# Kernel optimization log

Hardware: AMD Instinct MI355X
Metric: run time of the kernel (lower is better)

Reference implementation:

```python
import jax, jax.numpy as jnp
import numpy as np

INF = 100000000.0
TOPK = 27


def _box_iou(a, b):
    # a: [N,4] (x1,y1,x2,y2), b: [G,4] -> iou [N,G]
    area_a = (a[:, 2] - a[:, 0]) * (a[:, 3] - a[:, 1])
    area_b = (b[:, 2] - b[:, 0]) * (b[:, 3] - b[:, 1])
    lt = jnp.maximum(a[:, None, :2], b[None, :, :2])
    rb = jnp.minimum(a[:, None, 2:], b[None, :, 2:])
    wh = jnp.clip(rb - lt, 0.0)
    inter = wh[..., 0] * wh[..., 1]
    union = area_a[:, None] + area_b[None, :] - inter
    return inter / union, union


def _assign_one(anchors, gts, tokens):
    # anchors [N,4], gts [G,4], tokens [G,T]
    N = anchors.shape[0]
    G = gts.shape[0]
    ious, _ = _box_iou(anchors, gts)  # [N,G]

    a_cx = (anchors[:, 2] + anchors[:, 0]) * 0.5
    a_cy = (anchors[:, 3] + anchors[:, 1]) * 0.5
    g_cx = (gts[:, 2] + gts[:, 0]) * 0.5
    g_cy = (gts[:, 3] + gts[:, 1]) * 0.5

    # pairwise center distance [N,G]
    dist = jnp.sqrt((a_cx[:, None] - g_cx[None, :]) ** 2 +
                    (a_cy[:, None] - g_cy[None, :]) ** 2)

    # topk nearest anchors per gt (smallest distance) -> idxs [G,TOPK]
    _, topk_idxs = jax.lax.top_k(-dist.T, TOPK)

    # candidate ious [G,TOPK]
    cand = jnp.take_along_axis(ious.T, topk_idxs, axis=1)
    iou_mean = cand.mean(axis=1)
    iou_std = cand.std(axis=1, ddof=1)  # torch.std is unbiased
    is_pos = cand >= (iou_mean + iou_std)[:, None]

    # center-inside-gt check [G,TOPK]
    ax = a_cx[topk_idxs]
    ay = a_cy[topk_idxs]
    l = ax - gts[:, 0:1]
    t = ay - gts[:, 1:2]
    r = gts[:, 2:3] - ax
    b = gts[:, 3:4] - ay
    is_in_gts = jnp.minimum(jnp.minimum(l, t), jnp.minimum(r, b)) > 0.01
    is_pos = is_pos & is_in_gts

    # scatter candidate ious into flat [G*N] buffer of -INF (indices are unique)
    flat_idx = (jnp.arange(G)[:, None] * N + topk_idxs).reshape(-1)
    vals = ious.T.reshape(-1)[flat_idx]
    scat = jnp.where(is_pos.reshape(-1), vals, -INF)
    ious_inf = jnp.full((G * N,), -INF, dtype=ious.dtype).at[flat_idx].set(scat)
    ious_inf = ious_inf.reshape(G, N).T  # [N,G]

    anchors_to_gt_values = ious_inf.max(axis=1)          # [N]
    anchors_to_gt_indexs = ious_inf.argmax(axis=1)       # [N]

    matched_gts = gts[anchors_to_gt_indexs]              # [N,4]

    T = tokens.shape[1]
    unmatched = jnp.zeros((T,), tokens.dtype).at[-1].set(1.0)
    token_labels = jnp.where((anchors_to_gt_values == -INF)[:, None],
                             unmatched[None, :],
                             tokens[anchors_to_gt_indexs])  # [N,T]
    return anchors_to_gt_values, anchors_to_gt_indexs, matched_gts, token_labels


def setup_inputs() -> dict:
    key = jax.random.key(0)
    k1, k2, k3, k4, k5 = jax.random.split(key, 5)
    B, N, G, T = 8, 100000, 64, 256
    # anchors: valid x1<x2, y1<y2 boxes on a ~1024px canvas
    a_c = jax.random.uniform(k1, (B, N, 2), jnp.float32, 0.0, 1024.0)
    a_wh = jax.random.uniform(k2, (B, N, 2), jnp.float32, 8.0, 128.0)
    anchor_boxes = jnp.concatenate([a_c - a_wh / 2, a_c + a_wh / 2], axis=-1)
    g_c = jax.random.uniform(k3, (B, G, 2), jnp.float32, 0.0, 1024.0)
    g_wh = jax.random.uniform(k4, (B, G, 2), jnp.float32, 64.0, 512.0)
    gt_boxes = jnp.concatenate([g_c - g_wh / 2, g_c + g_wh / 2], axis=-1)
    token_map = jax.random.uniform(k5, (B, G, T), jnp.float32)
    return {"anchor_boxes": anchor_boxes, "gt_boxes": gt_boxes,
            "token_map": token_map}


def reference(anchor_boxes, gt_boxes, token_map):
    return jax.vmap(_assign_one)(anchor_boxes, gt_boxes, token_map)
```

## Files before the change

kernel.cpp:

```cpp
#include <hip/hip_runtime.h>
#include <cstdint>

constexpr int B = 8, N = 100000, G = 64, T = 256, TOPK = 27;
constexpr int BN = B * N;
constexpr int CAP = 2048;
constexpr int TOKEN_BLOCKS = 2048;
#define NEG_INF_VAL (-100000000.0f)

typedef float v4f __attribute__((ext_vector_type(4)));

__global__ __launch_bounds__(256) void atss_centers_kernel(
    const float* __restrict__ anchors, float2* __restrict__ ctr,
    unsigned long long* __restrict__ best)
{
#pragma clang fp contract(off)
  int i = blockIdx.x * 256 + threadIdx.x;
  if (i < BN) {
    float4 ab = ((const float4*)anchors)[i];
    ctr[i] = make_float2((ab.z + ab.x) * 0.5f, (ab.w + ab.y) * 0.5f);
    best[i] = 0ULL;
  }
}

__global__ __launch_bounds__(1024) void atss_assign_kernel(
    const float* __restrict__ anchors,
    const float2* __restrict__ ctr,
    const float* __restrict__ gts,
    unsigned long long* __restrict__ best)
{
#pragma clang fp contract(off)
  __shared__ float s_d[CAP];
  __shared__ int   s_i[CAP];
  __shared__ int   s_cnt;
  __shared__ int   s_sel[TOPK];
  __shared__ float s_iou[TOPK];
  __shared__ int   s_in[TOPK];
  __shared__ float s_thresh;

  const int bid = blockIdx.x;
  const int bg  = (bid & 7) * (B * G / 8) + (bid >> 3);
  const int b   = bg / G;
  const int g   = bg % G;
  const int tid = threadIdx.x;

  const float4 gbox = ((const float4*)gts)[bg];
  const float g_cx = (gbox.z + gbox.x) * 0.5f;
  const float g_cy = (gbox.w + gbox.y) * 0.5f;

  const float4*  abase = (const float4*)(anchors + (size_t)b * N * 4);
  const float2*  cbase = ctr + (size_t)b * N;
  const float4*  c4    = (const float4*)cbase;

  float thr2 = 24.0f * 24.0f;
  int M = 0;
  for (int attempt = 0; attempt < 8; ++attempt) {
    if (tid == 0) s_cnt = 0;
    __syncthreads();
    for (int m = tid; m < N / 4; m += 1024) {
      float4 ca = c4[2 * m];
      float4 cb = c4[2 * m + 1];
      float dx0 = ca.x - g_cx, dy0 = ca.y - g_cy;
      float d20 = __fmul_rn(dx0, dx0) + __fmul_rn(dy0, dy0);
      float dx1 = ca.z - g_cx, dy1 = ca.w - g_cy;
      float d21 = __fmul_rn(dx1, dx1) + __fmul_rn(dy1, dy1);
      float dx2 = cb.x - g_cx, dy2 = cb.y - g_cy;
      float d22 = __fmul_rn(dx2, dx2) + __fmul_rn(dy2, dy2);
      float dx3 = cb.z - g_cx, dy3 = cb.w - g_cy;
      float d23 = __fmul_rn(dx3, dx3) + __fmul_rn(dy3, dy3);
      if (d20 < thr2) {
        int p = atomicAdd(&s_cnt, 1);
        if (p < CAP) { s_d[p] = __fsqrt_rn(d20); s_i[p] = 4 * m; }
      }
      if (d21 < thr2) {
        int p = atomicAdd(&s_cnt, 1);
        if (p < CAP) { s_d[p] = __fsqrt_rn(d21); s_i[p] = 4 * m + 1; }
      }
      if (d22 < thr2) {
        int p = atomicAdd(&s_cnt, 1);
        if (p < CAP) { s_d[p] = __fsqrt_rn(d22); s_i[p] = 4 * m + 2; }
      }
      if (d23 < thr2) {
        int p = atomicAdd(&s_cnt, 1);
        if (p < CAP) { s_d[p] = __fsqrt_rn(d23); s_i[p] = 4 * m + 3; }
      }
    }
    __syncthreads();
    int cnt = s_cnt;
    __syncthreads();
    if (cnt >= TOPK && cnt <= CAP) { M = cnt; break; }
    thr2 = (cnt < TOPK) ? thr2 * 16.0f : thr2 * 0.25f;
  }

  for (int s = tid; s < M; s += 1024) {
    unsigned long long pk_s =
        ((unsigned long long)__float_as_uint(s_d[s]) << 20) |
        (unsigned long long)(unsigned)s_i[s];
    int rank = 0;
    for (int j = 0; j < M; ++j) {
      unsigned long long pk_j =
          ((unsigned long long)__float_as_uint(s_d[j]) << 20) |
          (unsigned long long)(unsigned)s_i[j];
      rank += (pk_j < pk_s) ? 1 : 0;
    }
    if (rank < TOPK) s_sel[rank] = s_i[s];
  }
  __syncthreads();

  if (tid < TOPK) {
    int a = s_sel[tid];
    float4 ab = abase[a];
    float area_a = __fmul_rn(ab.z - ab.x, ab.w - ab.y);
    float area_b = __fmul_rn(gbox.z - gbox.x, gbox.w - gbox.y);
    float ltx = fmaxf(ab.x, gbox.x), lty = fmaxf(ab.y, gbox.y);
    float rbx = fminf(ab.z, gbox.z), rby = fminf(ab.w, gbox.w);
    float w = fmaxf(rbx - ltx, 0.0f), h = fmaxf(rby - lty, 0.0f);
    float inter = __fmul_rn(w, h);
    float uni = (area_a + area_b) - inter;
    s_iou[tid] = inter / uni;
    float acx = (ab.z + ab.x) * 0.5f, acy = (ab.w + ab.y) * 0.5f;
    float l = acx - gbox.x, t = acy - gbox.y;
    float r = gbox.z - acx, bt = gbox.w - acy;
    float mn = fminf(fminf(l, t), fminf(r, bt));
    s_in[tid] = (mn > 0.01f) ? 1 : 0;
  }
  __syncthreads();

  if (tid == 0) {
    float sum = 0.0f;
    for (int k = 0; k < TOPK; ++k) sum += s_iou[k];
    float mean = sum / (float)TOPK;
    float vs = 0.0f;
    for (int k = 0; k < TOPK; ++k) {
      float d = s_iou[k] - mean;
      vs += __fmul_rn(d, d);
    }
    float sd = __fsqrt_rn(vs / (float)(TOPK - 1));
    s_thresh = mean + sd;
  }
  __syncthreads();

  if (tid < TOPK) {
    float iou = s_iou[tid];
    if (s_in[tid] && iou >= s_thresh) {
      unsigned long long pk =
          ((unsigned long long)__float_as_uint(iou) << 32) |
          (unsigned long long)(0xFFFFFFFFu - (unsigned)g);
      atomicMax(&best[(size_t)b * N + s_sel[tid]], pk);
    }
  }
}

__global__ __launch_bounds__(256) void atss_scalar_write_kernel(
    const unsigned long long* __restrict__ best,
    const float* __restrict__ gts,
    float* __restrict__ out)
{
  float* __restrict__ out_val = out;
  float* __restrict__ out_idx = out + (size_t)BN;
  float* __restrict__ out_mg  = out + (size_t)2 * BN;

  const int i = blockIdx.x * 256 + threadIdx.x;
  unsigned long long p = best[i];
  const int b_ = i / N;
  int g = 0;
  float val = NEG_INF_VAL;
  if (p != 0ULL) {
    g   = (int)(0xFFFFFFFFu - (unsigned)(p & 0xFFFFFFFFULL));
    val = __uint_as_float((unsigned)(p >> 32));
  }
  const int row = b_ * G + g;
  out_val[i] = val;
  out_idx[i] = (float)g;
  ((v4f*)out_mg)[i] = ((const v4f*)gts)[row];
}

__global__ __launch_bounds__(256) void atss_token_kernel(
    const unsigned long long* __restrict__ best,
    const float* __restrict__ tokens,
    float* __restrict__ out)
{
  float* __restrict__ out_tok = out + (size_t)6 * BN;
  const int lane = threadIdx.x & 63;
  const int NW   = TOKEN_BLOCKS * 4;
  int row = (blockIdx.x << 2) | (threadIdx.x >> 6);
  const v4f* tok4 = (const v4f*)tokens;

  unsigned long long p = best[row];
  while (true) {
    const int nrow = row + NW;
    unsigned long long pn = (nrow < BN) ? best[nrow] : 0ULL;
    v4f t;
    if (p != 0ULL) {
      const int b_ = row / N;
      const int g  = (int)(0xFFFFFFFFu - (unsigned)(p & 0xFFFFFFFFULL));
      t = tok4[(size_t)(b_ * G + g) * 64 + lane];
    } else {
      t = (v4f){0.0f, 0.0f, 0.0f, 0.0f};
      if (lane == 63) t.w = 1.0f;
    }
    ((v4f*)(out_tok + (size_t)row * T))[lane] = t;
    if (nrow >= BN) break;
    row = nrow;
    p = pn;
  }
}

extern "C" void kernel_launch(void* const* d_in, const int* in_sizes, int n_in,
                              void* d_out, int out_size, void* d_ws, size_t ws_size,
                              hipStream_t stream) {
  const float* anchors = (const float*)d_in[0];
  const float* gts     = (const float*)d_in[1];
  const float* tokens  = (const float*)d_in[2];
  float* out = (float*)d_out;

  unsigned long long* best = (unsigned long long*)d_ws;
  float2* ctr = (float2*)((char*)d_ws + sizeof(unsigned long long) * (size_t)BN);

  atss_centers_kernel<<<BN / 256, 256, 0, stream>>>(anchors, ctr, best);
  atss_assign_kernel<<<B * G, 1024, 0, stream>>>(anchors, ctr, gts, best);
  atss_scalar_write_kernel<<<BN / 256, 256, 0, stream>>>(best, gts, out);
  atss_token_kernel<<<TOKEN_BLOCKS, 256, 0, stream>>>(best, tokens, out);
}
```

Before: 846.5 us.

## Process two GT boxes per block to share anchor-center loads

Each assign block now handles two ground-truth boxes, scanning the anchor centers once and testing each center against both boxes, with separate candidate buffers and adaptive thresholds. This halves the number of center-array passes across the grid, cutting global memory traffic for the distance scan. In exchange the grid has only 256 blocks, fewer than the number of compute units, so parallelism drops. The per-box candidate capacity is reduced to fit two buffers in shared memory, which raises the chance of extra threshold retries.

```diff
diff --git a/kernel.cpp b/kernel.cpp
--- a/kernel.cpp
+++ b/kernel.cpp
@@ -3,7 +3,8 @@
 
 constexpr int B = 8, N = 100000, G = 64, T = 256, TOPK = 27;
 constexpr int BN = B * N;
-constexpr int CAP = 2048;
+constexpr int CAP = 1536;
+constexpr int GPB = 2;
 constexpr int TOKEN_BLOCKS = 2048;
 #define NEG_INF_VAL (-100000000.0f)
 
@@ -29,124 +30,142 @@
     unsigned long long* __restrict__ best)
 {
 #pragma clang fp contract(off)
-  __shared__ float s_d[CAP];
-  __shared__ int   s_i[CAP];
-  __shared__ int   s_cnt;
-  __shared__ int   s_sel[TOPK];
-  __shared__ float s_iou[TOPK];
-  __shared__ int   s_in[TOPK];
+  __shared__ float s_d[GPB][CAP];
+  __shared__ int   s_i[GPB][CAP];
+  __shared__ int   s_cnt[GPB];
+  __shared__ int   s_sel[GPB][TOPK];
+  __shared__ float s_iou[GPB][TOPK];
+  __shared__ int   s_in[GPB][TOPK];
   __shared__ float s_thresh;
 
   const int bid = blockIdx.x;
-  const int bg  = (bid & 7) * (B * G / 8) + (bid >> 3);
-  const int b   = bg / G;
-  const int g   = bg % G;
+  const int p   = (bid & 7) * 32 + (bid >> 3);
+  const int b   = p >> 5;
+  const int g0  = (p & 31) * 2;
+  const int bg0 = b * G + g0;
   const int tid = threadIdx.x;
 
-  const float4 gbox = ((const float4*)gts)[bg];
-  const float g_cx = (gbox.z + gbox.x) * 0.5f;
-  const float g_cy = (gbox.w + gbox.y) * 0.5f;
-
-  const float4*  abase = (const float4*)(anchors + (size_t)b * N * 4);
-  const float2*  cbase = ctr + (size_t)b * N;
-  const float4*  c4    = (const float4*)cbase;
-
-  float thr2 = 24.0f * 24.0f;
-  int M = 0;
-  for (int attempt = 0; attempt < 8; ++attempt) {
-    if (tid == 0) s_cnt = 0;
-    __syncthreads();
+  const float4 gb0 = ((const float4*)gts)[bg0];
+  const float4 gb1 = ((const float4*)gts)[bg0 + 1];
+  const float gcx0 = (gb0.z + gb0.x) * 0.5f, gcy0 = (gb0.w + gb0.y) * 0.5f;
+  const float gcx1 = (gb1.z + gb1.x) * 0.5f, gcy1 = (gb1.w + gb1.y) * 0.5f;
+
+  const float4* abase = (const float4*)(anchors + (size_t)b * N * 4);
+  const float4* c4    = (const float4*)(ctr + (size_t)b * N);
+
+  float thr2_0 = 576.0f, thr2_1 = 576.0f;
+  int M0 = -1, M1 = -1;
+  for (int attempt = 0; attempt < 8 && (M0 < 0 || M1 < 0); ++attempt) {
+    if (tid == 0 && M0 < 0) s_cnt[0] = 0;
+    if (tid == 1 && M1 < 0) s_cnt[1] = 0;
+    __syncthreads();
+    const bool a0 = (M0 < 0), a1 = (M1 < 0);
+
+#define ATSS_TEST(cx, cy, idx)                                                \
+  do {                                                                        \
+    if (a0) {                                                                 \
+      float dx = (cx) - gcx0, dy = (cy) - gcy0;                               \
+      float d2 = __fmul_rn(dx, dx) + __fmul_rn(dy, dy);                       \
+      if (d2 < thr2_0) {                                                      \
+        int q_ = atomicAdd(&s_cnt[0], 1);                                     \
+        if (q_ < CAP) { s_d[0][q_] = __fsqrt_rn(d2); s_i[0][q_] = (idx); }    \
+      }                                                                       \
+    }                                                                         \
+    if (a1) {                                                                 \
+      float dx = (cx) - gcx1, dy = (cy) - gcy1;                               \
+      float d2 = __fmul_rn(dx, dx) + __fmul_rn(dy, dy);                       \
+      if (d2 < thr2_1) {                                                      \
+        int q_ = atomicAdd(&s_cnt[1], 1);                                     \
+        if (q_ < CAP) { s_d[1][q_] = __fsqrt_rn(d2); s_i[1][q_] = (idx); }    \
+      }                                                                       \
+    }                                                                         \
+  } while (0)
+
     for (int m = tid; m < N / 4; m += 1024) {
       float4 ca = c4[2 * m];
       float4 cb = c4[2 * m + 1];
-      float dx0 = ca.x - g_cx, dy0 = ca.y - g_cy;
-      float d20 = __fmul_rn(dx0, dx0) + __fmul_rn(dy0, dy0);
-      float dx1 = ca.z - g_cx, dy1 = ca.w - g_cy;
-      float d21 = __fmul_rn(dx1, dx1) + __fmul_rn(dy1, dy1);
-      float dx2 = cb.x - g_cx, dy2 = cb.y - g_cy;
-      float d22 = __fmul_rn(dx2, dx2) + __fmul_rn(dy2, dy2);
-      float dx3 = cb.z - g_cx, dy3 = cb.w - g_cy;
-      float d23 = __fmul_rn(dx3, dx3) + __fmul_rn(dy3, dy3);
-      if (d20 < thr2) {
-        int p = atomicAdd(&s_cnt, 1);
-        if (p < CAP) { s_d[p] = __fsqrt_rn(d20); s_i[p] = 4 * m; }
+      ATSS_TEST(ca.x, ca.y, 4 * m);
+      ATSS_TEST(ca.z, ca.w, 4 * m + 1);
+      ATSS_TEST(cb.x, cb.y, 4 * m + 2);
+      ATSS_TEST(cb.z, cb.w, 4 * m + 3);
+    }
+#undef ATSS_TEST
+    __syncthreads();
+    const int c0 = s_cnt[0], c1 = s_cnt[1];
+    __syncthreads();
+    if (M0 < 0) {
+      if (c0 >= TOPK && c0 <= CAP) M0 = c0;
+      else thr2_0 *= (c0 < TOPK) ? 16.0f : 0.25f;
+    }
+    if (M1 < 0) {
+      if (c1 >= TOPK && c1 <= CAP) M1 = c1;
+      else thr2_1 *= (c1 < TOPK) ? 16.0f : 0.25f;
+    }
+  }
+
+  for (int q = 0; q < GPB; ++q) {
+    const int M = (q == 0) ? M0 : M1;
+    const float4 gbox = (q == 0) ? gb0 : gb1;
+    const int g = g0 + q;
+
+    for (int s = tid; s < M; s += 1024) {
+      unsigned long long pk_s =
+          ((unsigned long long)__float_as_uint(s_d[q][s]) << 20) |
+          (unsigned long long)(unsigned)s_i[q][s];
+      int rank = 0;
+      for (int j = 0; j < M; ++j) {
+        unsigned long long pk_j =
+            ((unsigned long long)__float_as_uint(s_d[q][j]) << 20) |
+            (unsigned long long)(unsigned)s_i[q][j];
+        rank += (pk_j < pk_s) ? 1 : 0;
       }
-      if (d21 < thr2) {
-        int p = atomicAdd(&s_cnt, 1);
-        if (p < CAP) { s_d[p] = __fsqrt_rn(d21); s_i[p] = 4 * m + 1; }
+      if (rank < TOPK) s_sel[q][rank] = s_i[q][s];
+    }
+    __syncthreads();
+
+    if (tid < TOPK) {
+      int a = s_sel[q][tid];
+      float4 ab = abase[a];
+      float area_a = __fmul_rn(ab.z - ab.x, ab.w - ab.y);
+      float area_b = __fmul_rn(gbox.z - gbox.x, gbox.w - gbox.y);
+      float ltx = fmaxf(ab.x, gbox.x), lty = fmaxf(ab.y, gbox.y);
+      float rbx = fminf(ab.z, gbox.z), rby = fminf(ab.w, gbox.w);
+      float w = fmaxf(rbx - ltx, 0.0f), h = fmaxf(rby - lty, 0.0f);
+      float inter = __fmul_rn(w, h);
+      float uni = (area_a + area_b) - inter;
+      s_iou[q][tid] = inter / uni;
+      float acx = (ab.z + ab.x) * 0.5f, acy = (ab.w + ab.y) * 0.5f;
+      float l = acx - gbox.x, t = acy - gbox.y;
+      float r = gbox.z - acx, bt = gbox.w - acy;
+      float mn = fminf(fminf(l, t), fminf(r, bt));
+      s_in[q][tid] = (mn > 0.01f) ? 1 : 0;
+    }
+    __syncthreads();
+
+    if (tid == 0) {
+      float sum = 0.0f;
+      for (int k = 0; k < TOPK; ++k) sum += s_iou[q][k];
+      float mean = sum / (float)TOPK;
+      float vs = 0.0f;
+      for (int k = 0; k < TOPK; ++k) {
+        float d = s_iou[q][k] - mean;
+        vs += __fmul_rn(d, d);
       }
-      if (d22 < thr2) {
-        int p = atomicAdd(&s_cnt, 1);
-        if (p < CAP) { s_d[p] = __fsqrt_rn(d22); s_i[p] = 4 * m + 2; }
+      float sd = __fsqrt_rn(vs / (float)(TOPK - 1));
+      s_thresh = mean + sd;
+    }
+    __syncthreads();
+
+    if (tid < TOPK) {
+      float iou = s_iou[q][tid];
+      if (s_in[q][tid] && iou >= s_thresh) {
+        unsigned long long pk =
+            ((unsigned long long)__float_as_uint(iou) << 32) |
+            (unsigned long long)(0xFFFFFFFFu - (unsigned)g);
+        atomicMax(&best[(size_t)b * N + s_sel[q][tid]], pk);
       }
-      if (d23 < thr2) {
-        int p = atomicAdd(&s_cnt, 1);
-        if (p < CAP) { s_d[p] = __fsqrt_rn(d23); s_i[p] = 4 * m + 3; }
-      }
-    }
-    __syncthreads();
-    int cnt = s_cnt;
-    __syncthreads();
-    if (cnt >= TOPK && cnt <= CAP) { M = cnt; break; }
-    thr2 = (cnt < TOPK) ? thr2 * 16.0f : thr2 * 0.25f;
-  }
-
-  for (int s = tid; s < M; s += 1024) {
-    unsigned long long pk_s =
-        ((unsigned long long)__float_as_uint(s_d[s]) << 20) |
-        (unsigned long long)(unsigned)s_i[s];
-    int rank = 0;
-    for (int j = 0; j < M; ++j) {
-      unsigned long long pk_j =
-          ((unsigned long long)__float_as_uint(s_d[j]) << 20) |
-          (unsigned long long)(unsigned)s_i[j];
-      rank += (pk_j < pk_s) ? 1 : 0;
-    }
-    if (rank < TOPK) s_sel[rank] = s_i[s];
-  }
-  __syncthreads();
-
-  if (tid < TOPK) {
-    int a = s_sel[tid];
-    float4 ab = abase[a];
-    float area_a = __fmul_rn(ab.z - ab.x, ab.w - ab.y);
-    float area_b = __fmul_rn(gbox.z - gbox.x, gbox.w - gbox.y);
-    float ltx = fmaxf(ab.x, gbox.x), lty = fmaxf(ab.y, gbox.y);
-    float rbx = fminf(ab.z, gbox.z), rby = fminf(ab.w, gbox.w);
-    float w = fmaxf(rbx - ltx, 0.0f), h = fmaxf(rby - lty, 0.0f);
-    float inter = __fmul_rn(w, h);
-    float uni = (area_a + area_b) - inter;
-    s_iou[tid] = inter / uni;
-    float acx = (ab.z + ab.x) * 0.5f, acy = (ab.w + ab.y) * 0.5f;
-    float l = acx - gbox.x, t = acy - gbox.y;
-    float r = gbox.z - acx, bt = gbox.w - acy;
-    float mn = fminf(fminf(l, t), fminf(r, bt));
-    s_in[tid] = (mn > 0.01f) ? 1 : 0;
-  }
-  __syncthreads();
-
-  if (tid == 0) {
-    float sum = 0.0f;
-    for (int k = 0; k < TOPK; ++k) sum += s_iou[k];
-    float mean = sum / (float)TOPK;
-    float vs = 0.0f;
-    for (int k = 0; k < TOPK; ++k) {
-      float d = s_iou[k] - mean;
-      vs += __fmul_rn(d, d);
-    }
-    float sd = __fsqrt_rn(vs / (float)(TOPK - 1));
-    s_thresh = mean + sd;
-  }
-  __syncthreads();
-
-  if (tid < TOPK) {
-    float iou = s_iou[tid];
-    if (s_in[tid] && iou >= s_thresh) {
-      unsigned long long pk =
-          ((unsigned long long)__float_as_uint(iou) << 32) |
-          (unsigned long long)(0xFFFFFFFFu - (unsigned)g);
-      atomicMax(&best[(size_t)b * N + s_sel[tid]], pk);
-    }
+    }
+    __syncthreads();
   }
 }
 
@@ -217,7 +236,7 @@
   float2* ctr = (float2*)((char*)d_ws + sizeof(unsigned long long) * (size_t)BN);
 
   atss_centers_kernel<<<BN / 256, 256, 0, stream>>>(anchors, ctr, best);
-  atss_assign_kernel<<<B * G, 1024, 0, stream>>>(anchors, ctr, gts, best);
+  atss_assign_kernel<<<B * G / GPB, 1024, 0, stream>>>(anchors, ctr, gts, best);
   atss_scalar_write_kernel<<<BN / 256, 256, 0, stream>>>(best, gts, out);
   atss_token_kernel<<<TOKEN_BLOCKS, 256, 0, stream>>>(best, tokens, out);
 }
```

After: 853.4 us. No clear change (+0.8%).
